# Kernel tuning notes

Hardware: AMD Instinct MI355X
Metric: run time of the kernel (lower is better)

## Reference

```python
import jax, jax.numpy as jnp
import numpy as np

B, C = 2048, 5000          # batchSize, classNum
LLR_REL = 0.9              # keep-rate; k = ceil(B*C*(1-llr_rel))
K = int(np.ceil(B * C * (1.0 - LLR_REL)))
MARGIN = 0.0


def _bce_with_logits(x, t):
    # elementwise BCEWithLogitsLoss (reduce=False): max(x,0) - x*t + log1p(exp(-|x|))
    return jnp.maximum(x, 0.0) - x * t + jnp.log1p(jnp.exp(-jnp.abs(x)))


def setup_inputs() -> dict:
    key = jax.random.key(0)
    k1, k2 = jax.random.split(key)
    inp = jax.random.normal(k1, (B, C), dtype=jnp.float32)
    # target in {-1, 0, +1}: -1 negative, 0 unobserved/ignored, +1 positive
    tgt = (jax.random.randint(k2, (B, C), 0, 3) - 1).astype(jnp.float32)
    return {"input": inp, "target": tgt, "k": K}


def reference(input, target, k):
    input = input.astype(jnp.float32)
    target = target.astype(jnp.float32)
    positive_mask = (target > MARGIN).astype(jnp.float32)
    negative_mask = (target < -MARGIN).astype(jnp.float32)
    positive_loss = _bce_with_logits(input, target)
    negative_loss = _bce_with_logits(-input, -target)
    unobserved_loss = negative_mask * negative_loss
    if k != 0:
        # k-th largest value of the flattened unobserved loss is the threshold
        topk_vals = jax.lax.top_k(unobserved_loss.reshape(-1), k)[0]
        topk_lossvalue = topk_vals[-1]
        loss_mask = (unobserved_loss < topk_lossvalue).astype(jnp.float32)
        negative_mask = negative_mask * loss_mask
    loss = positive_mask * positive_loss + negative_mask * negative_loss
    return loss
```

## Files before the change

### kernel.cpp

```cpp
#include <hip/hip_runtime.h>
#include <cstdint>
#include <cstddef>


struct SelState {
    uint32_t done;
    uint32_t prefix1;
    uint32_t k1rem;
    uint32_t u_kth;
    float    thr_nl;
};

#define GUARD 256u
#define HREP 8

__device__ __forceinline__ uint32_t xform(uint32_t b) {
    return ((int32_t)b < 0) ? ~b : (b | 0x80000000u);
}
__device__ __forceinline__ float unxform(uint32_t u) {
    uint32_t b = (u & 0x80000000u) ? (u ^ 0x80000000u) : ~u;
    return __uint_as_float(b);
}
__device__ __forceinline__ float neg_loss_precise(float x, float t) {
#pragma clang fp contract(off)
    return (fmaxf(-x, 0.0f) - x * t) + log1pf(expf(-fabsf(x)));
}

__device__ __forceinline__ void wscan(uint32_t m, int lane, uint32_t& excl, uint32_t& tot) {
    uint32_t inc = m;
#pragma unroll
    for (int d = 1; d < 64; d <<= 1) {
        uint32_t v = __shfl_up(inc, (unsigned)d, 64);
        if (lane >= d) inc += v;
    }
    excl = inc - m;
    tot = __shfl(inc, 63, 64);
}

__device__ __forceinline__ uint32_t quad_u_cls(uint32_t* my, float4 xv, float4 tv,
        uint32_t& u0, uint32_t& u1, uint32_t& u2, uint32_t& u3) {
    u0 = (tv.x < 0.0f) ? xform(__float_as_uint(xv.x)) : 0u;
    u1 = (tv.y < 0.0f) ? xform(__float_as_uint(xv.y)) : 0u;
    u2 = (tv.z < 0.0f) ? xform(__float_as_uint(xv.z)) : 0u;
    u3 = (tv.w < 0.0f) ? xform(__float_as_uint(xv.w)) : 0u;
    uint32_t cls = ((tv.x > 0.0f) ? 1u : ((tv.x < 0.0f) ? 2u : 0u))
                 | (((tv.y > 0.0f) ? 1u : ((tv.y < 0.0f) ? 2u : 0u)) << 2)
                 | (((tv.z > 0.0f) ? 1u : ((tv.z < 0.0f) ? 2u : 0u)) << 4)
                 | (((tv.w > 0.0f) ? 1u : ((tv.w < 0.0f) ? 2u : 0u)) << 6);
    if (u0) atomicAdd(&my[u0 >> 21], 1u);
    if (u1) atomicAdd(&my[u1 >> 21], 1u);
    if (u2) atomicAdd(&my[u2 >> 21], 1u);
    if (u3) atomicAdd(&my[u3 >> 21], 1u);
    return cls;
}

__global__ __launch_bounds__(256) void k1_hist(
        const float* __restrict__ x, const float* __restrict__ t,
        uint32_t* __restrict__ hrep, uint32_t* __restrict__ h21,
        uint32_t* __restrict__ cand1, uint32_t* __restrict__ wvcnt,
        uint8_t* __restrict__ cmap, int n, int segw) {
    const int S = gridDim.x * 256;
    const int gtid = blockIdx.x * 256 + threadIdx.x;

    {
        uint4* h4 = (uint4*)h21;
        uint4 z; z.x = 0u; z.y = 0u; z.z = 0u; z.w = 0u;
        for (int j = gtid; j < (1 << 19); j += S) h4[j] = z;
    }

    __shared__ uint32_t lh[2 * 2049];
    for (int j = threadIdx.x; j < 2 * 2049; j += 256) lh[j] = 0;
    __syncthreads();
    uint32_t* my = &lh[(threadIdx.x & 1) * 2049];

    const float4* x4 = (const float4*)x;
    const float4* t4 = (const float4*)t;
    const int n4 = n >> 2;
    const int lane = threadIdx.x & 63;
    const int wid  = threadIdx.x >> 6;
    uint32_t* wseg = cand1 + (size_t)(blockIdx.x * 4 + wid) * (size_t)segw;
    uint32_t wcur = 0;

    int M4 = 0;
    {
        long rem = (long)n4 - 1 - (long)(blockIdx.x * 256 + 255);
        if (rem >= 0) {
            long T = rem / S;
            if (T >= 3) M4 = (int)((T - 3) / 4 + 1);
        }
    }
    int i = blockIdx.x * 256 + threadIdx.x;

    for (int b = 0; b < M4; ++b, i += 4 * S) {
        float4 xa = x4[i], xb = x4[i + S], xc = x4[i + 2 * S], xd = x4[i + 3 * S];
        float4 ta = t4[i], tb = t4[i + S], tc = t4[i + 2 * S], td = t4[i + 3 * S];
        uint32_t u0, u1, u2, u3, u4_, u5, u6, u7, u8, u9, uA, uB, uC, uD, uE, uF;
        uint32_t ca = quad_u_cls(my, xa, ta, u0, u1, u2, u3);
        uint32_t cb = quad_u_cls(my, xb, tb, u4_, u5, u6, u7);
        uint32_t cc = quad_u_cls(my, xc, tc, u8, u9, uA, uB);
        uint32_t cd = quad_u_cls(my, xd, td, uC, uD, uE, uF);
        cmap[i]         = (uint8_t)ca;
        cmap[i + S]     = (uint8_t)cb;
        cmap[i + 2 * S] = (uint8_t)cc;
        cmap[i + 3 * S] = (uint8_t)cd;
        uint32_t m = (u0 != 0) + (u1 != 0) + (u2 != 0) + (u3 != 0)
                   + (u4_ != 0) + (u5 != 0) + (u6 != 0) + (u7 != 0)
                   + (u8 != 0) + (u9 != 0) + (uA != 0) + (uB != 0)
                   + (uC != 0) + (uD != 0) + (uE != 0) + (uF != 0);
        uint32_t excl, tot;
        wscan(m, lane, excl, tot);
        uint32_t p = wcur + excl;
        if (u0)  wseg[p++] = u0;
        if (u1)  wseg[p++] = u1;
        if (u2)  wseg[p++] = u2;
        if (u3)  wseg[p++] = u3;
        if (u4_) wseg[p++] = u4_;
        if (u5)  wseg[p++] = u5;
        if (u6)  wseg[p++] = u6;
        if (u7)  wseg[p++] = u7;
        if (u8)  wseg[p++] = u8;
        if (u9)  wseg[p++] = u9;
        if (uA)  wseg[p++] = uA;
        if (uB)  wseg[p++] = uB;
        if (uC)  wseg[p++] = uC;
        if (uD)  wseg[p++] = uD;
        if (uE)  wseg[p++] = uE;
        if (uF)  wseg[p++] = uF;
        wcur += tot;
    }

    for (; __any(i < n4); i += S) {
        const bool act = i < n4;
        float4 xa = act ? x4[i] : make_float4(0.f, 0.f, 0.f, 0.f);
        float4 ta = act ? t4[i] : make_float4(0.f, 0.f, 0.f, 0.f);
        uint32_t u0, u1, u2, u3;
        uint32_t ca = quad_u_cls(my, xa, ta, u0, u1, u2, u3);
        if (act) cmap[i] = (uint8_t)ca;
        uint32_t m = (u0 != 0) + (u1 != 0) + (u2 != 0) + (u3 != 0);
        uint32_t excl, tot;
        wscan(m, lane, excl, tot);
        uint32_t p = wcur + excl;
        if (u0) wseg[p++] = u0;
        if (u1) wseg[p++] = u1;
        if (u2) wseg[p++] = u2;
        if (u3) wseg[p++] = u3;
        wcur += tot;
    }

    if (blockIdx.x == 0) {
        int j = (n4 << 2) + threadIdx.x;
        const bool act = j < n;
        float xx = act ? x[j] : 0.0f;
        float tt = act ? t[j] : 0.0f;
        uint32_t u0 = (tt < 0.0f) ? xform(__float_as_uint(xx)) : 0u;
        if (u0) atomicAdd(&my[u0 >> 21], 1u);
        uint32_t excl, tot;
        wscan(u0 != 0 ? 1u : 0u, lane, excl, tot);
        if (u0) wseg[wcur + excl] = u0;
        wcur += tot;
    }

    if (lane == 0) wvcnt[blockIdx.x * 4 + wid] = wcur;

    __syncthreads();
    uint32_t* hmine = hrep + (size_t)(blockIdx.x & (HREP - 1)) * 2048;
    for (int b2 = threadIdx.x; b2 < 2048; b2 += 256) {
        uint32_t c = lh[b2] + lh[2049 + b2];
        if (c) atomicAdd(&hmine[b2], c);
    }
}

__global__ __launch_bounds__(256) void k2s(
        const uint32_t* __restrict__ hrep, const int* __restrict__ kptr,
        const uint32_t* __restrict__ cand1, const uint32_t* __restrict__ wvcnt,
        uint32_t* __restrict__ h21, SelState* __restrict__ st, int segw) {
    __shared__ uint32_t part[256];
    __shared__ uint32_t bc[2];
    const int tid = threadIdx.x;

    uint32_t cnt8[8];
    uint32_t lsum = 0;
#pragma unroll
    for (int j = 0; j < 8; ++j) {
        uint32_t c = 0;
#pragma unroll
        for (int r = 0; r < HREP; ++r) c += hrep[r * 2048 + tid * 8 + j];
        cnt8[j] = c;
        lsum += c;
    }
    part[tid] = lsum;
    __syncthreads();
    for (int off = 1; off < 256; off <<= 1) {
        uint32_t add = (tid + off < 256) ? part[tid + off] : 0u;
        __syncthreads();
        part[tid] += add;
        __syncthreads();
    }
    const uint32_t total = part[0];
    int kk = *kptr;
    uint32_t k = (kk > 0) ? (uint32_t)kk : 0u;
    if (k == 0u) {
        if (blockIdx.x == 0 && tid == 0) {
            st->done = 1u; st->u_kth = 0xFFFFFFFFu; st->thr_nl = __int_as_float(0x7F800000);
        }
        return;
    }
    if (k > total) {
        if (blockIdx.x == 0 && tid == 0) {
            st->done = 1u; st->u_kth = 0u; st->thr_nl = 0.0f;
        }
        return;
    }
    {
        uint32_t A = (tid < 255) ? part[tid + 1] : 0u;
#pragma unroll
        for (int j = 7; j >= 0; --j) {
            uint32_t c = cnt8[j];
            if (A < k && k <= A + c) {
                bc[0] = (uint32_t)(tid * 8 + j);
                bc[1] = k - A;
                if (blockIdx.x == 0) {
                    st->done = 0u;
                    st->prefix1 = (uint32_t)(tid * 8 + j);
                    st->k1rem = k - A;
                }
            }
            A += c;
        }
    }
    __syncthreads();
    const uint32_t prefix1 = bc[0];

    const int lane = tid & 63;
    const int wid  = tid >> 6;
    const int sidx = blockIdx.x * 4 + wid;
    const uint32_t cnt = wvcnt[sidx];
    const uint4* b4 = (const uint4*)(cand1 + (size_t)sidx * (size_t)segw);
    const uint32_t iters = (cnt + 255u) >> 8;
    for (uint32_t it = 0; it < iters; ++it) {
        const uint32_t e0 = it * 256u + (uint32_t)lane * 4u;
        uint4 v = b4[it * 64u + (uint32_t)lane];
        if (e0 + 0u < cnt && (v.x >> 21) == prefix1) atomicAdd(&h21[v.x & 0x1FFFFFu], 1u);
        if (e0 + 1u < cnt && (v.y >> 21) == prefix1) atomicAdd(&h21[v.y & 0x1FFFFFu], 1u);
        if (e0 + 2u < cnt && (v.z >> 21) == prefix1) atomicAdd(&h21[v.z & 0x1FFFFFu], 1u);
        if (e0 + 3u < cnt && (v.w >> 21) == prefix1) atomicAdd(&h21[v.w & 0x1FFFFFu], 1u);
    }
}

__global__ __launch_bounds__(256) void scan2a(
        const uint32_t* __restrict__ h21, uint32_t* __restrict__ csums) {
    __shared__ uint32_t red[256];
    const uint4* b4 = (const uint4*)(h21 + (size_t)blockIdx.x * 2048);
    uint32_t s = 0;
    for (int j = threadIdx.x; j < 512; j += 256) {
        uint4 v = b4[j];
        s += v.x + v.y + v.z + v.w;
    }
    red[threadIdx.x] = s;
    __syncthreads();
    for (int off = 128; off > 0; off >>= 1) {
        if (threadIdx.x < off) red[threadIdx.x] += red[threadIdx.x + off];
        __syncthreads();
    }
    if (threadIdx.x == 0) csums[blockIdx.x] = red[0];
}

__device__ __forceinline__ float fin1c(float xx, uint32_t cls, uint32_t ukth, float thr) {
    float lp = __logf(1.0f + __expf(-fabsf(xx)));
    float v = 0.0f;
    if (cls == 1u) {
        v = (fmaxf(xx, 0.0f) - xx) + lp;
    } else if (cls == 2u) {
        uint32_t u = xform(__float_as_uint(xx));
        bool keep = u < ukth;
        if (keep && (ukth - u) < GUARD)
            keep = neg_loss_precise(xx, -1.0f) < thr;
        if (keep) v = (fmaxf(-xx, 0.0f) + xx) + lp;
    }
    return v;
}
__device__ __forceinline__ float4 fin_quadc(float4 xv, uint32_t cb, uint32_t ukth, float thr) {
    float4 r;
    r.x = fin1c(xv.x, cb & 3u, ukth, thr);
    r.y = fin1c(xv.y, (cb >> 2) & 3u, ukth, thr);
    r.z = fin1c(xv.z, (cb >> 4) & 3u, ukth, thr);
    r.w = fin1c(xv.w, (cb >> 6) & 3u, ukth, thr);
    return r;
}
__device__ __forceinline__ float fin1t(float xx, float tt, uint32_t ukth, float thr) {
    float lp = __logf(1.0f + __expf(-fabsf(xx)));
    float v = 0.0f;
    if (tt > 0.0f) {
        v = fmaxf(xx, 0.0f) - xx * tt + lp;
    } else if (tt < 0.0f) {
        uint32_t u = xform(__float_as_uint(xx));
        bool keep = u < ukth;
        if (keep && (ukth - u) < GUARD)
            keep = neg_loss_precise(xx, tt) < thr;
        if (keep) v = fmaxf(-xx, 0.0f) - xx * tt + lp;
    }
    return v;
}

__global__ __launch_bounds__(256) void kf(
        const float* __restrict__ x, const float* __restrict__ t,
        const uint8_t* __restrict__ cmap, const uint32_t* __restrict__ h21,
        const uint32_t* __restrict__ csums, const SelState* __restrict__ st,
        float* __restrict__ out, int n) {
    __shared__ uint32_t part[256];
    __shared__ uint32_t bc[4];
    __shared__ uint32_t s_done, s_pref1, s_k1rem, s_ukth, s_thr;
    const int tid = threadIdx.x;
    if (tid == 0) {
        s_done = st->done;  s_pref1 = st->prefix1;  s_k1rem = st->k1rem;
        s_ukth = st->u_kth; s_thr = __float_as_uint(st->thr_nl);
    }
    __syncthreads();

    uint32_t ukth;
    float thr;
    if (s_done) {
        ukth = s_ukth;
        thr = __uint_as_float(s_thr);
    } else {
        const uint32_t k = s_k1rem;
        uint32_t c4v[4];
        uint32_t lsum = 0;
#pragma unroll
        for (int j = 0; j < 4; ++j) { c4v[j] = csums[tid * 4 + j]; lsum += c4v[j]; }
        part[tid] = lsum;
        __syncthreads();
        for (int off = 1; off < 256; off <<= 1) {
            uint32_t add = (tid + off < 256) ? part[tid + off] : 0u;
            __syncthreads();
            part[tid] += add;
            __syncthreads();
        }
        uint32_t A = (tid < 255) ? part[tid + 1] : 0u;
#pragma unroll
        for (int j = 3; j >= 0; --j) {
            uint32_t c = c4v[j];
            if (A < k && k <= A + c) { bc[0] = (uint32_t)(tid * 4 + j); bc[1] = k - A; }
            A += c;
        }
        __syncthreads();
        const uint32_t chunk = bc[0];
        const uint32_t k2 = bc[1];
        __syncthreads();

        const uint32_t* base = h21 + (size_t)chunk * 2048;
        uint32_t b8[8];
        lsum = 0;
#pragma unroll
        for (int j = 0; j < 8; ++j) { b8[j] = base[tid * 8 + j]; lsum += b8[j]; }
        part[tid] = lsum;
        __syncthreads();
        for (int off = 1; off < 256; off <<= 1) {
            uint32_t add = (tid + off < 256) ? part[tid + off] : 0u;
            __syncthreads();
            part[tid] += add;
            __syncthreads();
        }
        A = (tid < 255) ? part[tid + 1] : 0u;
#pragma unroll
        for (int j = 7; j >= 0; --j) {
            uint32_t c = b8[j];
            if (A < k2 && k2 <= A + c) {
                uint32_t u = (s_pref1 << 21) | (chunk * 2048u + (uint32_t)(tid * 8 + j));
                bc[2] = u;
                bc[3] = __float_as_uint(neg_loss_precise(unxform(u), -1.0f));
            }
            A += c;
        }
        __syncthreads();
        ukth = bc[2];
        thr = __uint_as_float(bc[3]);
    }

    const float4* x4 = (const float4*)x;
    float4* o4 = (float4*)out;
    const int n4 = n >> 2;
    const int S = gridDim.x * 256;
    int i = blockIdx.x * 256 + tid;
    for (; i + 3 * S < n4; i += 4 * S) {
        float4 xa = x4[i], xb = x4[i + S], xc = x4[i + 2 * S], xd = x4[i + 3 * S];
        uint32_t ca = cmap[i], cb = cmap[i + S], cc = cmap[i + 2 * S], cd = cmap[i + 3 * S];
        o4[i]         = fin_quadc(xa, ca, ukth, thr);
        o4[i + S]     = fin_quadc(xb, cb, ukth, thr);
        o4[i + 2 * S] = fin_quadc(xc, cc, ukth, thr);
        o4[i + 3 * S] = fin_quadc(xd, cd, ukth, thr);
    }
    for (; i < n4; i += S) {
        float4 xa = x4[i];
        uint32_t ca = cmap[i];
        o4[i] = fin_quadc(xa, ca, ukth, thr);
    }
    if (blockIdx.x == 0) {
        for (int j = (n4 << 2) + tid; j < n; j += 256) {
            out[j] = fin1t(x[j], t[j], ukth, thr);
        }
    }
}

extern "C" void kernel_launch(void* const* d_in, const int* in_sizes, int n_in,
                              void* d_out, int out_size, void* d_ws, size_t ws_size,
                              hipStream_t stream) {
    const float* x = (const float*)d_in[0];
    const float* t = (const float*)d_in[1];
    const int* kptr = (const int*)d_in[2];
    float* out = (float*)d_out;
    const int n = in_sizes[0];
    if (n <= 0) return;

    const int n4 = n >> 2;
    int work = (n4 + 255) / 256;
    if (work < 1) work = 1;
    int grid = work < 1024 ? work : 1024;
    const int S = grid * 256;
    const int Q = (n4 + S - 1) / S;
    const int segw = 256 * Q + 4;

    char* ws = (char*)d_ws;
    uint32_t* hrep  = (uint32_t*)(ws + 0);
    SelState* st    = (SelState*)(ws + 65536);
    uint32_t* h21   = (uint32_t*)(ws + 65792);
    size_t csoff = 65792 + ((size_t)1u << 21) * 4u;
    uint32_t* csums = (uint32_t*)(ws + csoff);
    uint32_t* wvcnt = (uint32_t*)(ws + csoff + 4096);
    size_t cmoff = csoff + 4096 + 16384;
    uint8_t*  cmap  = (uint8_t*)(ws + cmoff);
    size_t c1off = (cmoff + (size_t)n4 + 255) & ~(size_t)255;
    uint32_t* cand1 = (uint32_t*)(ws + c1off);

    hipMemsetAsync(d_ws, 0, 65536, stream);

    k1_hist<<<grid, 256, 0, stream>>>(x, t, hrep, h21, cand1, wvcnt, cmap, n, segw);
    k2s    <<<grid, 256, 0, stream>>>(hrep, kptr, cand1, wvcnt, h21, st, segw);
    scan2a <<<1024, 256, 0, stream>>>(h21, csums);
    kf     <<<grid, 256, 0, stream>>>(x, t, cmap, h21, csums, st, out, n);
}
```

Before: 164.4 us.

## Fuse coarse chunk-sum histogram into k2s and drop scan2a kernel

While scattering the second-level radix counts into the 2M-bin h21 histogram, k2s also builds a 1024-bin coarse histogram (bits 11..20) in shared memory. It flushes this into 8 replicated global copies. The final kernel sums those replicas instead of reading chunk sums from a separate scan2a pass. This removes one kernel launch and a full 8 MB read of h21, at the cost of extra LDS atomics per candidate and a larger memset.

```diff
diff --git a/kernel.cpp b/kernel.cpp
--- a/kernel.cpp
+++ b/kernel.cpp
@@ -173,10 +173,14 @@
 __global__ __launch_bounds__(256) void k2s(
         const uint32_t* __restrict__ hrep, const int* __restrict__ kptr,
         const uint32_t* __restrict__ cand1, const uint32_t* __restrict__ wvcnt,
-        uint32_t* __restrict__ h21, SelState* __restrict__ st, int segw) {
+        uint32_t* __restrict__ h21, uint32_t* __restrict__ hcoarse,
+        SelState* __restrict__ st, int segw) {
     __shared__ uint32_t part[256];
     __shared__ uint32_t bc[2];
+    __shared__ uint32_t chist[2 * 1025];
     const int tid = threadIdx.x;
+
+    for (int j = tid; j < 2 * 1025; j += 256) chist[j] = 0;
 
     uint32_t cnt8[8];
     uint32_t lsum = 0;
@@ -230,6 +234,7 @@
     }
     __syncthreads();
     const uint32_t prefix1 = bc[0];
+    uint32_t* mych = &chist[(tid & 1) * 1025];
 
     const int lane = tid & 63;
     const int wid  = tid >> 6;
@@ -240,29 +245,29 @@
     for (uint32_t it = 0; it < iters; ++it) {
         const uint32_t e0 = it * 256u + (uint32_t)lane * 4u;
         uint4 v = b4[it * 64u + (uint32_t)lane];
-        if (e0 + 0u < cnt && (v.x >> 21) == prefix1) atomicAdd(&h21[v.x & 0x1FFFFFu], 1u);
-        if (e0 + 1u < cnt && (v.y >> 21) == prefix1) atomicAdd(&h21[v.y & 0x1FFFFFu], 1u);
-        if (e0 + 2u < cnt && (v.z >> 21) == prefix1) atomicAdd(&h21[v.z & 0x1FFFFFu], 1u);
-        if (e0 + 3u < cnt && (v.w >> 21) == prefix1) atomicAdd(&h21[v.w & 0x1FFFFFu], 1u);
-    }
-}
-
-__global__ __launch_bounds__(256) void scan2a(
-        const uint32_t* __restrict__ h21, uint32_t* __restrict__ csums) {
-    __shared__ uint32_t red[256];
-    const uint4* b4 = (const uint4*)(h21 + (size_t)blockIdx.x * 2048);
-    uint32_t s = 0;
-    for (int j = threadIdx.x; j < 512; j += 256) {
-        uint4 v = b4[j];
-        s += v.x + v.y + v.z + v.w;
-    }
-    red[threadIdx.x] = s;
-    __syncthreads();
-    for (int off = 128; off > 0; off >>= 1) {
-        if (threadIdx.x < off) red[threadIdx.x] += red[threadIdx.x + off];
-        __syncthreads();
-    }
-    if (threadIdx.x == 0) csums[blockIdx.x] = red[0];
+        if (e0 + 0u < cnt && (v.x >> 21) == prefix1) {
+            atomicAdd(&h21[v.x & 0x1FFFFFu], 1u);
+            atomicAdd(&mych[(v.x >> 11) & 1023u], 1u);
+        }
+        if (e0 + 1u < cnt && (v.y >> 21) == prefix1) {
+            atomicAdd(&h21[v.y & 0x1FFFFFu], 1u);
+            atomicAdd(&mych[(v.y >> 11) & 1023u], 1u);
+        }
+        if (e0 + 2u < cnt && (v.z >> 21) == prefix1) {
+            atomicAdd(&h21[v.z & 0x1FFFFFu], 1u);
+            atomicAdd(&mych[(v.z >> 11) & 1023u], 1u);
+        }
+        if (e0 + 3u < cnt && (v.w >> 21) == prefix1) {
+            atomicAdd(&h21[v.w & 0x1FFFFFu], 1u);
+            atomicAdd(&mych[(v.w >> 11) & 1023u], 1u);
+        }
+    }
+    __syncthreads();
+    uint32_t* cmine = hcoarse + (size_t)(blockIdx.x & (HREP - 1)) * 1024;
+    for (int b2 = tid; b2 < 1024; b2 += 256) {
+        uint32_t c = chist[b2] + chist[1025 + b2];
+        if (c) atomicAdd(&cmine[b2], c);
+    }
 }
 
 __device__ __forceinline__ float fin1c(float xx, uint32_t cls, uint32_t ukth, float thr) {
@@ -305,7 +310,7 @@
 __global__ __launch_bounds__(256) void kf(
         const float* __restrict__ x, const float* __restrict__ t,
         const uint8_t* __restrict__ cmap, const uint32_t* __restrict__ h21,
-        const uint32_t* __restrict__ csums, const SelState* __restrict__ st,
+        const uint32_t* __restrict__ hcoarse, const SelState* __restrict__ st,
         float* __restrict__ out, int n) {
     __shared__ uint32_t part[256];
     __shared__ uint32_t bc[4];
@@ -327,7 +332,13 @@
         uint32_t c4v[4];
         uint32_t lsum = 0;
 #pragma unroll
-        for (int j = 0; j < 4; ++j) { c4v[j] = csums[tid * 4 + j]; lsum += c4v[j]; }
+        for (int j = 0; j < 4; ++j) {
+            uint32_t c = 0;
+#pragma unroll
+            for (int r = 0; r < HREP; ++r) c += hcoarse[r * 1024 + tid * 4 + j];
+            c4v[j] = c;
+            lsum += c;
+        }
         part[tid] = lsum;
         __syncthreads();
         for (int off = 1; off < 256; off <<= 1) {
@@ -421,21 +432,20 @@
     const int segw = 256 * Q + 4;
 
     char* ws = (char*)d_ws;
-    uint32_t* hrep  = (uint32_t*)(ws + 0);
-    SelState* st    = (SelState*)(ws + 65536);
-    uint32_t* h21   = (uint32_t*)(ws + 65792);
-    size_t csoff = 65792 + ((size_t)1u << 21) * 4u;
-    uint32_t* csums = (uint32_t*)(ws + csoff);
-    uint32_t* wvcnt = (uint32_t*)(ws + csoff + 4096);
-    size_t cmoff = csoff + 4096 + 16384;
-    uint8_t*  cmap  = (uint8_t*)(ws + cmoff);
+    uint32_t* hrep    = (uint32_t*)(ws + 0);
+    uint32_t* hcoarse = (uint32_t*)(ws + 65536);
+    SelState* st      = (SelState*)(ws + 98304);
+    uint32_t* h21     = (uint32_t*)(ws + 98560);
+    size_t wvoff = 98560 + ((size_t)1u << 21) * 4u;
+    uint32_t* wvcnt   = (uint32_t*)(ws + wvoff);
+    size_t cmoff = wvoff + 16384;
+    uint8_t*  cmap    = (uint8_t*)(ws + cmoff);
     size_t c1off = (cmoff + (size_t)n4 + 255) & ~(size_t)255;
-    uint32_t* cand1 = (uint32_t*)(ws + c1off);
-
-    hipMemsetAsync(d_ws, 0, 65536, stream);
+    uint32_t* cand1   = (uint32_t*)(ws + c1off);
+
+    hipMemsetAsync(d_ws, 0, 98560, stream);
 
     k1_hist<<<grid, 256, 0, stream>>>(x, t, hrep, h21, cand1, wvcnt, cmap, n, segw);
-    k2s    <<<grid, 256, 0, stream>>>(hrep, kptr, cand1, wvcnt, h21, st, segw);
-    scan2a <<<1024, 256, 0, stream>>>(h21, csums);
-    kf     <<<grid, 256, 0, stream>>>(x, t, cmap, h21, csums, st, out, n);
-}
+    k2s    <<<grid, 256, 0, stream>>>(hrep, kptr, cand1, wvcnt, h21, hcoarse, st, segw);
+    kf     <<<grid, 256, 0, stream>>>(x, t, cmap, h21, hcoarse, st, out, n);
+}
```

Result: no change. 162.4 us (-1.2%).
